# Optimization experiments

Hardware: AMD Instinct MI355X
Metric: run time of the kernel (lower is better)

Reference implementation:

```python
import jax, jax.numpy as jnp
import numpy as np

EMBED = 512
HEADS = 8
HEAD_DIM = EMBED // HEADS


def setup_inputs() -> dict:
    key = jax.random.key(0)
    ks = jax.random.split(key, 8)
    N, S = 4, 2048
    values = jax.random.normal(ks[0], (N, S, EMBED), dtype=jnp.float32)
    keys = jax.random.normal(ks[1], (N, S, EMBED), dtype=jnp.float32)
    query = jax.random.normal(ks[2], (N, S, EMBED), dtype=jnp.float32)
    mask = jnp.ones((N, 1, 1, S), dtype=jnp.int32)
    # per-head projection weights (nn.Linear: y = x @ W.T), no bias
    Wv = jax.random.normal(ks[3], (HEAD_DIM, HEAD_DIM), dtype=jnp.float32) / np.sqrt(HEAD_DIM)
    Wk = jax.random.normal(ks[4], (HEAD_DIM, HEAD_DIM), dtype=jnp.float32) / np.sqrt(HEAD_DIM)
    Wq = jax.random.normal(ks[5], (HEAD_DIM, HEAD_DIM), dtype=jnp.float32) / np.sqrt(HEAD_DIM)
    Wo = jax.random.normal(ks[6], (EMBED, EMBED), dtype=jnp.float32) / np.sqrt(EMBED)
    bo = jax.random.normal(ks[7], (EMBED,), dtype=jnp.float32) * 0.01
    return {"values": values, "keys": keys, "query": query, "mask": mask,
            "Wv": Wv, "Wk": Wk, "Wq": Wq, "Wo": Wo, "bo": bo}


def reference(values, keys, query, mask, Wv, Wk, Wq, Wo, bo):
    N, S, _ = query.shape
    scale = jnp.sqrt(jnp.float32(HEAD_DIM))
    v = values.reshape(N, S, HEADS, HEAD_DIM) @ Wv.T
    k = keys.reshape(N, S, HEADS, HEAD_DIM) @ Wk.T
    q = query.reshape(N, S, HEADS, HEAD_DIM) @ Wq.T
    energy = jnp.einsum('nqhd,nkhd->nhqk', q, k) / scale  # [N,H,S,S]
    energy = jnp.where(mask == 0, jnp.float32(-1e20), energy)
    attn = jax.nn.softmax(energy, axis=3)
    # dropout is identity in eval mode
    out = jnp.einsum('nhql,nlhd->nqhd', attn, v).reshape(N, S, EMBED)
    return out @ Wo.T + bo
```

## Files before the change

### kernel.cpp

```cpp
#include <hip/hip_runtime.h>
#include <hip/hip_bf16.h>

#define EMB 512
#define NHEADS 8
#define HD 64
#define SEQ 2048

typedef float f32x4 __attribute__((ext_vector_type(4)));
typedef float f32x16 __attribute__((ext_vector_type(16)));
typedef short short8 __attribute__((ext_vector_type(8)));
typedef unsigned short ushort4_t __attribute__((ext_vector_type(4)));
typedef unsigned uint2v __attribute__((ext_vector_type(2)));

#define MFMA(a, b, c)   __builtin_amdgcn_mfma_f32_16x16x32_bf16((a), (b), (c), 0, 0, 0)
#define MFMA32(a, b, c) __builtin_amdgcn_mfma_f32_32x32x16_bf16((a), (b), (c), 0, 0, 0)

__device__ inline unsigned short f2bf(float f) {
    union { float f; unsigned u; } v; v.f = f;
    unsigned r = v.u + 0x7fffu + ((v.u >> 16) & 1u);
    return (unsigned short)(r >> 16);
}

__device__ inline unsigned cvt_pk_bf16(float a, float b) {
    unsigned r;
    asm("v_cvt_pk_bf16_f32 %0, %1, %2" : "=v"(r) : "v"(a), "v"(b));
    return r;
}

__device__ inline void plswap(unsigned &a, unsigned &b) {
#if __has_builtin(__builtin_amdgcn_permlane32_swap)
    uint2v r = __builtin_amdgcn_permlane32_swap(a, b, false, false);
    a = r[0]; b = r[1];
#else
    asm volatile("v_permlane32_swap_b32 %0, %1" : "+v"(a), "+v"(b));
#endif
}

__device__ inline short8 mk8(unsigned a, unsigned b, unsigned c, unsigned d) {
    union { unsigned u[4]; short8 s; } x;
    x.u[0] = a; x.u[1] = b; x.u[2] = c; x.u[3] = d;
    return x.s;
}

__device__ inline short8 f8_to_bf8(float4 a, float4 b) {
    short8 r;
    r[0] = (short)f2bf(a.x); r[1] = (short)f2bf(a.y);
    r[2] = (short)f2bf(a.z); r[3] = (short)f2bf(a.w);
    r[4] = (short)f2bf(b.x); r[5] = (short)f2bf(b.y);
    r[6] = (short)f2bf(b.z); r[7] = (short)f2bf(b.w);
    return r;
}

__global__ __launch_bounds__(256) void qkv_proj_kernel(
    const float* __restrict__ vin, const float* __restrict__ kin,
    const float* __restrict__ qin, const unsigned short* __restrict__ wqkvb,
    unsigned short* __restrict__ q_ws, unsigned short* __restrict__ k_ws,
    unsigned short* __restrict__ vt_ws)
{
    const int z = blockIdx.y;
    const float* __restrict__ x = (z == 0) ? qin : (z == 1 ? kin : vin);
    const unsigned short* __restrict__ wb = wqkvb + z * HD * HD;

    const int bid = blockIdx.x;
    const int st = bid & 15;
    const int h  = (bid >> 4) & 7;
    const int n  = bid >> 7;

    const int lane = threadIdx.x & 63;
    const int w    = threadIdx.x >> 6;
    const int lo = lane & 15, hi = lane >> 4;
    const int s_base = st * 128 + w * 32;

    short8 b[2][4];
#pragma unroll
    for (int nb = 0; nb < 4; ++nb)
#pragma unroll
        for (int kb = 0; kb < 2; ++kb)
            b[kb][nb] = *(const short8*)(wb + (lo + 16 * nb) * HD + kb * 32 + hi * 8);

    short8 a[2][2];
#pragma unroll
    for (int sub = 0; sub < 2; ++sub) {
        const float* xr = x + ((size_t)n * SEQ + s_base + 16 * sub + lo) * EMB + h * HD;
#pragma unroll
        for (int kb = 0; kb < 2; ++kb) {
            const float4* p = (const float4*)(xr + kb * 32 + hi * 8);
            a[sub][kb] = f8_to_bf8(p[0], p[1]);
        }
    }

    f32x4 acc[2][4];
#pragma unroll
    for (int sub = 0; sub < 2; ++sub)
#pragma unroll
        for (int nb = 0; nb < 4; ++nb) {
            f32x4 t = {0.f, 0.f, 0.f, 0.f};
            t = MFMA(a[sub][0], b[0][nb], t);
            t = MFMA(a[sub][1], b[1][nb], t);
            acc[sub][nb] = t;
        }

    const size_t nh = (size_t)n * NHEADS + h;
    if (z < 2) {
        const float sc = (z == 0) ? 0.18033688011112042f : 1.0f;
        unsigned short* o = (z == 0 ? q_ws : k_ws) + nh * SEQ * HD;
#pragma unroll
        for (int sub = 0; sub < 2; ++sub)
#pragma unroll
            for (int nb = 0; nb < 4; ++nb)
#pragma unroll
                for (int i = 0; i < 4; ++i)
                    o[(size_t)(s_base + 16 * sub + hi * 4 + i) * HD + lo + 16 * nb] =
                        f2bf(acc[sub][nb][i] * sc);
    } else {
        unsigned short* o = vt_ws + nh * HD * SEQ;
#pragma unroll
        for (int sub = 0; sub < 2; ++sub)
#pragma unroll
            for (int nb = 0; nb < 4; ++nb) {
                ushort4_t pk;
                pk[0] = f2bf(acc[sub][nb][0]); pk[1] = f2bf(acc[sub][nb][1]);
                pk[2] = f2bf(acc[sub][nb][2]); pk[3] = f2bf(acc[sub][nb][3]);
                *(ushort4_t*)(o + (size_t)(lo + 16 * nb) * SEQ + s_base + 16 * sub + hi * 4) = pk;
            }
    }
}

__global__ __launch_bounds__(256) void prep_kernel(
    const float* __restrict__ Wo, unsigned short* __restrict__ wob,
    const float* __restrict__ Wq, const float* __restrict__ Wk,
    const float* __restrict__ Wv, unsigned short* __restrict__ wqkvb,
    const int* __restrict__ mask, unsigned* __restrict__ flags)
{
    const int b = blockIdx.x;
    if (b < 128) {
        const int idx = (b * 256 + threadIdx.x) * 8;
        const float4* p = (const float4*)(Wo + idx);
        *(short8*)(wob + idx) = f8_to_bf8(p[0], p[1]);
    } else if (b < 134) {
        const int idx = ((b - 128) * 256 + threadIdx.x) * 8;
        const float* src = (idx < 4096) ? (Wq + idx)
                         : (idx < 8192) ? (Wk + idx - 4096)
                                        : (Wv + idx - 8192);
        const float4* p = (const float4*)src;
        *(short8*)(wqkvb + idx) = f8_to_bf8(p[0], p[1]);
    } else {
        const int n = b - 134;
        const int t = threadIdx.x;
        if (t < 64) {
            bool has0 = false;
            if (t < 32) {
                const int* mrow = mask + (size_t)n * SEQ + t * 64;
#pragma unroll 4
                for (int j = 0; j < 64; j += 4) {
                    int4 m4 = *(const int4*)(mrow + j);
                    has0 |= (m4.x == 0) | (m4.y == 0) | (m4.z == 0) | (m4.w == 0);
                }
            }
            unsigned long long bl = __ballot(has0);
            if (t == 0) flags[n] = (unsigned)(bl & 0xffffffffu);
        }
    }
}

__global__ __launch_bounds__(512, 1) void attn_kernel(
    const unsigned short* __restrict__ q_ws, const unsigned short* __restrict__ k_ws,
    const unsigned short* __restrict__ vt_ws, const int* __restrict__ mask,
    const unsigned* __restrict__ flags, unsigned short* __restrict__ ao_ws)
{
    __shared__ __align__(16) unsigned short klds[64][72];
    __shared__ __align__(16) unsigned short vlds[64][72];
    __shared__ __align__(16) int            mlds[64];
    __shared__ __align__(16) float          llds[8][32];

    const int tid  = threadIdx.x;
    const int lane = tid & 63;
    const int w    = tid >> 6;
    const int l31  = lane & 31;
    const int hi5  = lane >> 5;
    const int bid = (blockIdx.x & 7) * 32 + (blockIdx.x >> 3);
    const int wid = bid * 8 + w;
    const int qb  = wid & 63;
    const int h   = (wid >> 6) & 7;
    const int n   = wid >> 9;
    const size_t nh = (size_t)n * NHEADS + h;

    const unsigned short* qp = q_ws + nh * SEQ * HD;
    const unsigned short* kp = k_ws + nh * SEQ * HD;
    const unsigned short* vp = vt_ws + nh * HD * SEQ;
    const int* mp = mask + (size_t)n * SEQ;
    const unsigned fl = flags[n];

    const int q0 = qb * 32;
    short8 bq[4];
#pragma unroll
    for (int s = 0; s < 4; ++s)
        bq[s] = *(const short8*)(qp + (size_t)(q0 + l31) * HD + 16 * s + 8 * hi5);

    f32x16 o0, o1;
#pragma unroll
    for (int r = 0; r < 16; ++r) { o0[r] = 0.f; o1[r] = 0.f; }
    float lacc = 0.f;

    const int sr = tid >> 3;
    const int sc = (tid & 7) * 8;
    short8 rk = *(const short8*)(kp + (size_t)sr * HD + sc);
    short8 rv = *(const short8*)(vp + (size_t)sr * SEQ + sc);
    int    rm = (w == 0) ? mp[lane] : 0;

    for (int t = 0; t < 32; ++t) {
        const int kt = t * 64;
        __syncthreads();
        *(short8*)(&klds[sr][sc]) = rk;
        *(short8*)(&vlds[sr][sc]) = rv;
        if (w == 0) mlds[lane] = rm;
        __syncthreads();

        if (t < 31) {
            const int ktn = kt + 64;
            rk = *(const short8*)(kp + (size_t)(ktn + sr) * HD + sc);
            rv = *(const short8*)(vp + (size_t)sr * SEQ + ktn + sc);
            rm = (w == 0) ? mp[ktn + lane] : 0;
        }

        const bool masked = (fl >> t) & 1u;
        short8 pa[4];
#pragma unroll
        for (int kb = 0; kb < 2; ++kb) {
            f32x16 e;
#pragma unroll
            for (int r = 0; r < 16; ++r) e[r] = 0.f;
#pragma unroll
            for (int s = 0; s < 4; ++s) {
                short8 ak = *(const short8*)(&klds[32 * kb + l31][16 * s + 8 * hi5]);
                e = MFMA32(ak, bq[s], e);
            }
            if (masked) {
#pragma unroll
                for (int r = 0; r < 16; ++r) {
                    const int key = 32 * kb + (r & 3) + 8 * (r >> 2) + 4 * hi5;
                    if (mlds[key] == 0) e[r] = -1e30f;
                }
            }
            unsigned wv[8];
#pragma unroll
            for (int r2 = 0; r2 < 8; ++r2) {
                float p0 = __builtin_amdgcn_exp2f(e[2 * r2]);
                float p1 = __builtin_amdgcn_exp2f(e[2 * r2 + 1]);
                lacc += p0 + p1;
                wv[r2] = cvt_pk_bf16(p0, p1);
            }
            plswap(wv[0], wv[2]); plswap(wv[1], wv[3]);
            plswap(wv[4], wv[6]); plswap(wv[5], wv[7]);
            pa[2 * kb]     = mk8(wv[0], wv[1], wv[2], wv[3]);
            pa[2 * kb + 1] = mk8(wv[4], wv[5], wv[6], wv[7]);
        }
#pragma unroll
        for (int s = 0; s < 4; ++s) {
            short8 bv0 = *(const short8*)(&vlds[l31][16 * s + 8 * hi5]);
            short8 bv1 = *(const short8*)(&vlds[32 + l31][16 * s + 8 * hi5]);
            o0 = MFMA32(pa[s], bv0, o0);
            o1 = MFMA32(pa[s], bv1, o1);
        }
    }

    lacc += __shfl_xor(lacc, 32);
    if (lane < 32) llds[w][lane] = 1.0f / lacc;

    unsigned short* op = ao_ws + ((size_t)n * SEQ + q0) * EMB + h * HD;
#pragma unroll
    for (int r = 0; r < 16; ++r) {
        const int qrow = (r & 3) + 8 * (r >> 2) + 4 * hi5;
        const float linv = llds[w][qrow];
        op[(size_t)qrow * EMB + l31]      = f2bf(o0[r] * linv);
        op[(size_t)qrow * EMB + 32 + l31] = f2bf(o1[r] * linv);
    }
}

__global__ __launch_bounds__(256) void out_proj_kernel(
    const unsigned short* __restrict__ ao_ws, const unsigned short* __restrict__ wob,
    const float* __restrict__ bo, float* __restrict__ out)
{
    const int swz = (blockIdx.x & 7) * 64 + (blockIdx.x >> 3);
    const int nc = swz & 7;
    const int mt = swz >> 3;
    const int lane = threadIdx.x & 63;
    const int w = threadIdx.x >> 6;
    const int lo = lane & 15, hi = lane >> 4;
    const int m0 = mt * 128 + w * 32;
    const int e0 = nc * 64;

    f32x4 acc[2][4];
#pragma unroll
    for (int sub = 0; sub < 2; ++sub)
#pragma unroll
        for (int nb = 0; nb < 4; ++nb)
            acc[sub][nb] = (f32x4){0.f, 0.f, 0.f, 0.f};

    const unsigned short* ar0 = ao_ws + (size_t)(m0 + lo) * EMB;
    const unsigned short* ar1 = ao_ws + (size_t)(m0 + 16 + lo) * EMB;
    for (int k0 = 0; k0 < EMB; k0 += 32) {
        short8 a0 = *(const short8*)(ar0 + k0 + hi * 8);
        short8 a1 = *(const short8*)(ar1 + k0 + hi * 8);
#pragma unroll
        for (int nb = 0; nb < 4; ++nb) {
            short8 b = *(const short8*)(wob + (size_t)(e0 + lo + 16 * nb) * EMB + k0 + hi * 8);
            acc[0][nb] = MFMA(a0, b, acc[0][nb]);
            acc[1][nb] = MFMA(a1, b, acc[1][nb]);
        }
    }
#pragma unroll
    for (int sub = 0; sub < 2; ++sub)
#pragma unroll
        for (int nb = 0; nb < 4; ++nb) {
            float bias = bo[e0 + lo + 16 * nb];
#pragma unroll
            for (int i = 0; i < 4; ++i)
                out[(size_t)(m0 + 16 * sub + hi * 4 + i) * EMB + e0 + lo + 16 * nb] =
                    acc[sub][nb][i] + bias;
        }
}

extern "C" void kernel_launch(void* const* d_in, const int* in_sizes, int n_in,
                              void* d_out, int out_size, void* d_ws, size_t ws_size,
                              hipStream_t stream)
{
    const float* vin = (const float*)d_in[0];
    const float* kin = (const float*)d_in[1];
    const float* qin = (const float*)d_in[2];
    const int*  mask = (const int*)d_in[3];
    const float* Wv  = (const float*)d_in[4];
    const float* Wk  = (const float*)d_in[5];
    const float* Wq  = (const float*)d_in[6];
    const float* Wo  = (const float*)d_in[7];
    const float* bo  = (const float*)d_in[8];
    float* out = (float*)d_out;

    const int N = in_sizes[0] / (SEQ * EMB);

    char* ws = (char*)d_ws;
    const size_t qkv_bytes = (size_t)N * NHEADS * SEQ * HD * 2;
    unsigned short* q_ws  = (unsigned short*)(ws);
    unsigned short* k_ws  = (unsigned short*)(ws + qkv_bytes);
    unsigned short* vt_ws = (unsigned short*)(ws + 2 * qkv_bytes);
    unsigned short* ao_ws = (unsigned short*)(ws + 3 * qkv_bytes);
    unsigned short* wob   = (unsigned short*)(ws + 4 * qkv_bytes);
    unsigned*       flags = (unsigned*)(ws + 4 * qkv_bytes + (size_t)EMB * EMB * 2);
    unsigned short* wqkvb = (unsigned short*)(ws + 4 * qkv_bytes + (size_t)EMB * EMB * 2 + 4096);

    hipLaunchKernelGGL(prep_kernel, dim3(134 + N), dim3(256), 0, stream,
                       Wo, wob, Wq, Wk, Wv, wqkvb, mask, flags);
    hipLaunchKernelGGL(qkv_proj_kernel, dim3(N * NHEADS * (SEQ / 128), 3), dim3(256), 0, stream,
                       vin, kin, qin, wqkvb, q_ws, k_ws, vt_ws);
    hipLaunchKernelGGL(attn_kernel, dim3(N * NHEADS * (SEQ / 32) / 8), dim3(512), 0, stream,
                       q_ws, k_ws, vt_ws, mask, flags, ao_ws);
    hipLaunchKernelGGL(out_proj_kernel, dim3((N * SEQ / 128) * (EMB / 64)), dim3(256), 0, stream,
                       ao_ws, wob, bo, out);
}
```

Measured before the change: 90.53 us.

## Split key tile across wave pairs in attention and reduce partial outputs in LDS

Each wave now processes 64 queries (two 32-row blocks) against only half of each 64-key tile. Wave pairs split the keys and combine their partial output accumulators and row sums through shared memory at the end. The aim is to halve the per-wave LDS reads of K and V fragments, since each loaded fragment is reused across two query blocks. In exchange it adds a 64KB float LDS reduction buffer, an extra barrier and epilogue, and more accumulator registers per wave.

After: 91.02 us. Within noise of the previous version (+0.5%).

```diff
diff --git a/kernel.cpp b/kernel.cpp
--- a/kernel.cpp
+++ b/kernel.cpp
@@ -171,18 +171,21 @@
     __shared__ __align__(16) unsigned short klds[64][72];
     __shared__ __align__(16) unsigned short vlds[64][72];
     __shared__ __align__(16) int            mlds[64];
-    __shared__ __align__(16) float          llds[8][32];
+    __shared__ __align__(16) float          llds[4][2][32];
+    __shared__ __align__(16) float          lhalf[4][2][32];
+    __shared__               float          olds[4][64][64];
 
     const int tid  = threadIdx.x;
     const int lane = tid & 63;
     const int w    = tid >> 6;
+    const int g    = w & 3;
+    const int kh   = w >> 2;
     const int l31  = lane & 31;
     const int hi5  = lane >> 5;
     const int bid = (blockIdx.x & 7) * 32 + (blockIdx.x >> 3);
-    const int wid = bid * 8 + w;
-    const int qb  = wid & 63;
-    const int h   = (wid >> 6) & 7;
-    const int n   = wid >> 9;
+    const int qt  = bid & 7;
+    const int h   = (bid >> 3) & 7;
+    const int n   = bid >> 6;
     const size_t nh = (size_t)n * NHEADS + h;
 
     const unsigned short* qp = q_ws + nh * SEQ * HD;
@@ -191,16 +194,23 @@
     const int* mp = mask + (size_t)n * SEQ;
     const unsigned fl = flags[n];
 
-    const int q0 = qb * 32;
-    short8 bq[4];
-#pragma unroll
-    for (int s = 0; s < 4; ++s)
-        bq[s] = *(const short8*)(qp + (size_t)(q0 + l31) * HD + 16 * s + 8 * hi5);
-
-    f32x16 o0, o1;
-#pragma unroll
-    for (int r = 0; r < 16; ++r) { o0[r] = 0.f; o1[r] = 0.f; }
-    float lacc = 0.f;
+    const int qbase = qt * 256 + 64 * g;
+    short8 bq[2][4];
+#pragma unroll
+    for (int qi = 0; qi < 2; ++qi)
+#pragma unroll
+        for (int s = 0; s < 4; ++s)
+            bq[qi][s] = *(const short8*)(qp + (size_t)(qbase + 32 * qi + l31) * HD
+                                         + 16 * s + 8 * hi5);
+
+    f32x16 o[2][2];
+#pragma unroll
+    for (int qi = 0; qi < 2; ++qi)
+#pragma unroll
+        for (int db = 0; db < 2; ++db)
+#pragma unroll
+            for (int r = 0; r < 16; ++r) o[qi][db][r] = 0.f;
+    float lacc[2] = {0.f, 0.f};
 
     const int sr = tid >> 3;
     const int sc = (tid & 7) * 8;
@@ -223,22 +233,31 @@
             rm = (w == 0) ? mp[ktn + lane] : 0;
         }
 
+        short8 ak[4];
+#pragma unroll
+        for (int s = 0; s < 4; ++s)
+            ak[s] = *(const short8*)(&klds[32 * kh + l31][16 * s + 8 * hi5]);
+        short8 bv[2][2];
+#pragma unroll
+        for (int db = 0; db < 2; ++db)
+#pragma unroll
+            for (int sp = 0; sp < 2; ++sp)
+                bv[db][sp] = *(const short8*)(&vlds[32 * db + l31]
+                                              [16 * (2 * kh + sp) + 8 * hi5]);
+
         const bool masked = (fl >> t) & 1u;
-        short8 pa[4];
-#pragma unroll
-        for (int kb = 0; kb < 2; ++kb) {
+#pragma unroll
+        for (int qi = 0; qi < 2; ++qi) {
             f32x16 e;
 #pragma unroll
             for (int r = 0; r < 16; ++r) e[r] = 0.f;
 #pragma unroll
-            for (int s = 0; s < 4; ++s) {
-                short8 ak = *(const short8*)(&klds[32 * kb + l31][16 * s + 8 * hi5]);
-                e = MFMA32(ak, bq[s], e);
-            }
+            for (int s = 0; s < 4; ++s)
+                e = MFMA32(ak[s], bq[qi][s], e);
             if (masked) {
 #pragma unroll
                 for (int r = 0; r < 16; ++r) {
-                    const int key = 32 * kb + (r & 3) + 8 * (r >> 2) + 4 * hi5;
+                    const int key = 32 * kh + (r & 3) + 8 * (r >> 2) + 4 * hi5;
                     if (mlds[key] == 0) e[r] = -1e30f;
                 }
             }
@@ -247,33 +266,62 @@
             for (int r2 = 0; r2 < 8; ++r2) {
                 float p0 = __builtin_amdgcn_exp2f(e[2 * r2]);
                 float p1 = __builtin_amdgcn_exp2f(e[2 * r2 + 1]);
-                lacc += p0 + p1;
+                lacc[qi] += p0 + p1;
                 wv[r2] = cvt_pk_bf16(p0, p1);
             }
             plswap(wv[0], wv[2]); plswap(wv[1], wv[3]);
             plswap(wv[4], wv[6]); plswap(wv[5], wv[7]);
-            pa[2 * kb]     = mk8(wv[0], wv[1], wv[2], wv[3]);
-            pa[2 * kb + 1] = mk8(wv[4], wv[5], wv[6], wv[7]);
-        }
-#pragma unroll
-        for (int s = 0; s < 4; ++s) {
-            short8 bv0 = *(const short8*)(&vlds[l31][16 * s + 8 * hi5]);
-            short8 bv1 = *(const short8*)(&vlds[32 + l31][16 * s + 8 * hi5]);
-            o0 = MFMA32(pa[s], bv0, o0);
-            o1 = MFMA32(pa[s], bv1, o1);
-        }
-    }
-
-    lacc += __shfl_xor(lacc, 32);
-    if (lane < 32) llds[w][lane] = 1.0f / lacc;
-
-    unsigned short* op = ao_ws + ((size_t)n * SEQ + q0) * EMB + h * HD;
-#pragma unroll
-    for (int r = 0; r < 16; ++r) {
-        const int qrow = (r & 3) + 8 * (r >> 2) + 4 * hi5;
-        const float linv = llds[w][qrow];
-        op[(size_t)qrow * EMB + l31]      = f2bf(o0[r] * linv);
-        op[(size_t)qrow * EMB + 32 + l31] = f2bf(o1[r] * linv);
+            short8 paA = mk8(wv[0], wv[1], wv[2], wv[3]);
+            short8 paB = mk8(wv[4], wv[5], wv[6], wv[7]);
+            o[qi][0] = MFMA32(paA, bv[0][0], o[qi][0]);
+            o[qi][0] = MFMA32(paB, bv[0][1], o[qi][0]);
+            o[qi][1] = MFMA32(paA, bv[1][0], o[qi][1]);
+            o[qi][1] = MFMA32(paB, bv[1][1], o[qi][1]);
+        }
+    }
+
+    lacc[0] += __shfl_xor(lacc[0], 32);
+    lacc[1] += __shfl_xor(lacc[1], 32);
+
+    if (kh == 1) {
+#pragma unroll
+        for (int qi = 0; qi < 2; ++qi)
+#pragma unroll
+            for (int db = 0; db < 2; ++db)
+#pragma unroll
+                for (int r = 0; r < 16; ++r)
+                    olds[g][qi * 32 + db * 16 + r][lane] = o[qi][db][r];
+        if (lane < 32) {
+            lhalf[g][0][l31] = lacc[0];
+            lhalf[g][1][l31] = lacc[1];
+        }
+    }
+    __syncthreads();
+    if (kh == 0) {
+#pragma unroll
+        for (int qi = 0; qi < 2; ++qi)
+#pragma unroll
+            for (int db = 0; db < 2; ++db)
+#pragma unroll
+                for (int r = 0; r < 16; ++r)
+                    o[qi][db][r] += olds[g][qi * 32 + db * 16 + r][lane];
+        lacc[0] += lhalf[g][0][l31];
+        lacc[1] += lhalf[g][1][l31];
+        if (lane < 32) {
+            llds[g][0][l31] = 1.0f / lacc[0];
+            llds[g][1][l31] = 1.0f / lacc[1];
+        }
+#pragma unroll
+        for (int qi = 0; qi < 2; ++qi) {
+            unsigned short* op = ao_ws + ((size_t)n * SEQ + qbase + 32 * qi) * EMB + h * HD;
+#pragma unroll
+            for (int r = 0; r < 16; ++r) {
+                const int qrow = (r & 3) + 8 * (r >> 2) + 4 * hi5;
+                const float linv = llds[g][qi][qrow];
+                op[(size_t)qrow * EMB + l31]      = f2bf(o[qi][0][r] * linv);
+                op[(size_t)qrow * EMB + 32 + l31] = f2bf(o[qi][1][r] * linv);
+            }
+        }
     }
 }
 
@@ -352,7 +400,7 @@
                        Wo, wob, Wq, Wk, Wv, wqkvb, mask, flags);
     hipLaunchKernelGGL(qkv_proj_kernel, dim3(N * NHEADS * (SEQ / 128), 3), dim3(256), 0, stream,
                        vin, kin, qin, wqkvb, q_ws, k_ws, vt_ws);
-    hipLaunchKernelGGL(attn_kernel, dim3(N * NHEADS * (SEQ / 32) / 8), dim3(512), 0, stream,
+    hipLaunchKernelGGL(attn_kernel, dim3(N * NHEADS * (SEQ / 256)), dim3(512), 0, stream,
                        q_ws, k_ws, vt_ws, mask, flags, ao_ws);
     hipLaunchKernelGGL(out_proj_kernel, dim3((N * SEQ / 128) * (EMB / 64)), dim3(256), 0, stream,
                        ao_ws, wob, bo, out);
```
